# Performance work log

Measured on AMD Instinct MI355X. Metric: run time of the kernel, lower is better.

The kernel has to match this reference:

```python
import jax, jax.numpy as jnp
import numpy as np

B, S, E, H = 2, 2048, 1024, 16
HD = E // H

def setup_inputs() -> dict:
    key = jax.random.key(0)
    ks = jax.random.split(key, 9)
    s = 1.0 / np.sqrt(E)
    inp = {
        'x': jax.random.normal(ks[0], (B, S, E), dtype=jnp.float32),
        'Wq': jax.random.uniform(ks[1], (E, E), jnp.float32, -s, s),
        'bq': jax.random.uniform(ks[2], (E,), jnp.float32, -s, s),
        'Wk': jax.random.uniform(ks[3], (E, E), jnp.float32, -s, s),
        'bk': jax.random.uniform(ks[4], (E,), jnp.float32, -s, s),
        'Wv': jax.random.uniform(ks[5], (E, E), jnp.float32, -s, s),
        'bv': jax.random.uniform(ks[6], (E,), jnp.float32, -s, s),
        'Wo': jax.random.uniform(ks[7], (E, E), jnp.float32, -s, s),
        'bo': jax.random.uniform(ks[8], (E,), jnp.float32, -s, s),
    }
    return inp

def reference(x, Wq, bq, Wk, bk, Wv, bv, Wo, bo):
    # Linear layers: y = x @ W^T + b (torch nn.Linear convention)
    q = x @ Wq.T + bq  # [B,S,E]
    k = x @ Wk.T + bk
    v = x @ Wv.T + bv
    q = q.reshape(B, S, H, HD).transpose(0, 2, 1, 3)  # [B,H,S,hd]
    k = k.reshape(B, S, H, HD).transpose(0, 2, 1, 3)
    v = v.reshape(B, S, H, HD).transpose(0, 2, 1, 3)
    scores = jnp.einsum('bhqd,bhkd->bhqk', q, k) / jnp.sqrt(jnp.float32(HD))
    attn = jax.nn.softmax(scores, axis=-1)
    out = jnp.einsum('bhqk,bhkd->bhqd', attn, v)  # [B,H,S,hd]
    out = out.transpose(0, 2, 1, 3).reshape(B, S, E)
    return out @ Wo.T + bo
```

## Files before the change

### kernel.cpp

```cpp
#include <hip/hip_runtime.h>
#include <hip/hip_bf16.h>

#define B_ 2
#define S_ 2048
#define E_ 1024
#define H_ 16
#define HD_ 64
#define M_ (B_ * S_)

typedef __attribute__((ext_vector_type(8))) short bf16x8;
typedef __attribute__((ext_vector_type(4))) float f32x4;
typedef __attribute__((ext_vector_type(4))) unsigned short u16x4;
typedef unsigned short ushort_t;

static __device__ __forceinline__ ushort_t f2bf(float f) {
    union { __hip_bfloat16 b; ushort_t u; } cv;
    cv.b = __float2bfloat16(f);
    return cv.u;
}
static __device__ __forceinline__ float bf2f(ushort_t u) {
    union { unsigned int i; float f; } cv;
    cv.i = ((unsigned int)u) << 16;
    return cv.f;
}
static __device__ __forceinline__ void gl2lds16(const ushort_t* g, ushort_t* l) {
    __builtin_amdgcn_global_load_lds(
        (const __attribute__((address_space(1))) unsigned int*)g,
        (__attribute__((address_space(3))) unsigned int*)l,
        16, 0, 0);
}

__global__ __launch_bounds__(256)
void conv_pack(const float* __restrict__ x,  const float* __restrict__ Wq,
               const float* __restrict__ Wk, const float* __restrict__ Wv,
               const float* __restrict__ Wo, const float* __restrict__ bq,
               const float* __restrict__ bk, const float* __restrict__ bv,
               ushort_t* __restrict__ xb,  ushort_t* __restrict__ Wqb,
               ushort_t* __restrict__ Wkb, ushort_t* __restrict__ Wvb,
               ushort_t* __restrict__ Wohi, ushort_t* __restrict__ Wolo,
               float* __restrict__ bcat)
{
    const int NX = (B_ * S_ * E_) / 4;
    const int NW = (E_ * E_) / 4;
    const int total = NX + 4 * NW + 768;
    for (int u = blockIdx.x * blockDim.x + threadIdx.x; u < total;
         u += gridDim.x * blockDim.x) {
        if (u < NX) {
            float4 v = ((const float4*)x)[u];
            u16x4 o = { f2bf(v.x), f2bf(v.y), f2bf(v.z), f2bf(v.w) };
            ((u16x4*)xb)[u] = o;
        } else if (u < NX + 3 * NW) {
            int r = (u - NX) >> 18;
            int i = (u - NX) & (NW - 1);
            const float* src = (r == 0) ? Wq : ((r == 1) ? Wk : Wv);
            ushort_t*    dst = (r == 0) ? Wqb : ((r == 1) ? Wkb : Wvb);
            float4 v = ((const float4*)src)[i];
            u16x4 o = { f2bf(v.x), f2bf(v.y), f2bf(v.z), f2bf(v.w) };
            ((u16x4*)dst)[i] = o;
        } else if (u < NX + 4 * NW) {
            int i = u - NX - 3 * NW;
            float4 v = ((const float4*)Wo)[i];
            u16x4 hv, lv;
            float vv[4] = { v.x, v.y, v.z, v.w };
            #pragma unroll
            for (int r = 0; r < 4; ++r) {
                ushort_t hb = f2bf(vv[r]);
                hv[r] = hb;
                lv[r] = f2bf(vv[r] - bf2f(hb));
            }
            ((u16x4*)Wohi)[i] = hv;
            ((u16x4*)Wolo)[i] = lv;
        } else {
            int i = u - NX - 4 * NW;
            int r = i >> 8, ii = i & 255;
            const float* src = (r == 0) ? bq : ((r == 1) ? bk : bv);
            ((float4*)bcat)[r * 256 + ii] = ((const float4*)src)[ii];
        }
    }
}

template<int MODE>
__global__ __launch_bounds__(256)
void gemm_mfma(const ushort_t* __restrict__ Aa, const ushort_t* __restrict__ Ab,
               const ushort_t* __restrict__ W0p, const ushort_t* __restrict__ W1p,
               const ushort_t* __restrict__ W2p, const float* __restrict__ bias,
               ushort_t* __restrict__ O0, ushort_t* __restrict__ O1,
               ushort_t* __restrict__ O2, float* __restrict__ Of)
{
    constexpr int NBX = MODE ? 16 : 48;
    constexpr int NT  = MODE ? 48 : 16;
    __shared__ ushort_t As[2][128 * 64];
    __shared__ ushort_t Ws[2][64 * 64];

    const int nwg = NBX * (M_ / 128);
    const int b0  = blockIdx.x;
    const int bid = (b0 & 7) * (nwg >> 3) + (b0 >> 3);
    const int bx = bid % NBX, by = bid / NBX;
    const int m0 = by * 128, n0 = bx * 64;

    const int t = threadIdx.x;
    const int w = t >> 6, lane = t & 63;
    const int g = lane >> 4, qi = lane & 15, sw = qi & 7;
    const int wr = w >> 1, wc = w & 1;

    const ushort_t* WA;
    int nw0;
    int region = 0;
    if (MODE == 0) {
        region = n0 >> 10;
        WA = (region == 0) ? W0p : (region == 1) ? W1p : W2p;
        nw0 = n0 & 1023;
    } else {
        WA = W0p;
        nw0 = n0;
    }

    auto stage = [&](int buf, int kt) {
        const ushort_t *Acur, *Wcur;
        if (MODE == 0) { Acur = Aa; Wcur = WA; }
        else {
            int pass = kt >> 4;
            Acur = (pass == 2) ? Ab : Aa;
            Wcur = (pass == 1) ? W1p : W0p;
        }
        const int k0 = (MODE ? (kt & 15) : kt) * 64;
        #pragma unroll
        for (int it = 0; it < 4; ++it) {
            int idx = (it * 4 + w) * 64 + lane;
            int row = idx >> 3, c8 = idx & 7;
            gl2lds16(&Acur[(size_t)(m0 + row) * E_ + k0 + ((c8 ^ (row & 7)) << 3)],
                     &As[buf][(it * 4 + w) * 512]);
        }
        #pragma unroll
        for (int it = 0; it < 2; ++it) {
            int idx = (it * 4 + w) * 64 + lane;
            int row = idx >> 3, c8 = idx & 7;
            gl2lds16(&Wcur[(size_t)(nw0 + row) * E_ + k0 + ((c8 ^ (row & 7)) << 3)],
                     &Ws[buf][(it * 4 + w) * 512]);
        }
    };

    f32x4 acc[4][2];
    #pragma unroll
    for (int i = 0; i < 4; ++i)
        #pragma unroll
        for (int j = 0; j < 2; ++j) acc[i][j] = (f32x4){0.f, 0.f, 0.f, 0.f};

    stage(0, 0);
    __syncthreads();

    for (int kt = 0; kt < NT; ++kt) {
        const int cur = kt & 1;
        if (kt + 1 < NT) stage(cur ^ 1, kt + 1);
        #pragma unroll
        for (int h = 0; h < 2; ++h) {
            bf16x8 af[4], wf[2];
            #pragma unroll
            for (int i = 0; i < 4; ++i)
                af[i] = *(const bf16x8*)&As[cur][(wr * 64 + i * 16 + qi) * 64 +
                                                 (((h * 4 + g) ^ sw) << 3)];
            #pragma unroll
            for (int j = 0; j < 2; ++j)
                wf[j] = *(const bf16x8*)&Ws[cur][(wc * 32 + j * 16 + qi) * 64 +
                                                 (((h * 4 + g) ^ sw) << 3)];
            __builtin_amdgcn_s_setprio(1);
            #pragma unroll
            for (int i = 0; i < 4; ++i)
                #pragma unroll
                for (int j = 0; j < 2; ++j)
                    acc[i][j] = __builtin_amdgcn_mfma_f32_16x16x32_bf16(
                        af[i], wf[j], acc[i][j], 0, 0, 0);
            __builtin_amdgcn_s_setprio(0);
        }
        __syncthreads();
    }

    if (MODE == 0) {
        ushort_t* Out = (region == 0) ? O0 : (region == 1) ? O1 : O2;
        const float oscale = (region == 0) ? 0.18033688f : 1.0f;
        const int hh = (n0 & 1023) >> 6;
        #pragma unroll
        for (int j = 0; j < 2; ++j) {
            const int n = n0 + wc * 32 + j * 16 + qi;
            const int d = n & 63;
            const float bj = bias[n];
            #pragma unroll
            for (int i = 0; i < 4; ++i)
                #pragma unroll
                for (int r = 0; r < 4; ++r) {
                    const int m = m0 + wr * 64 + i * 16 + g * 4 + r;
                    const int b = m >> 11, s = m & (S_ - 1);
                    Out[(((size_t)(b * H_ + hh)) * S_ + s) * HD_ + d] =
                        f2bf((acc[i][j][r] + bj) * oscale);
                }
        }
    } else {
        #pragma unroll
        for (int j = 0; j < 2; ++j) {
            const int n = n0 + wc * 32 + j * 16 + qi;
            const float bj = bias[n];
            #pragma unroll
            for (int i = 0; i < 4; ++i)
                #pragma unroll
                for (int r = 0; r < 4; ++r) {
                    const int m = m0 + wr * 64 + i * 16 + g * 4 + r;
                    Of[(size_t)m * E_ + n] = acc[i][j][r] + bj;
                }
        }
    }
}

__global__ __launch_bounds__(256)
void attn_mfma(const ushort_t* __restrict__ Qg, const ushort_t* __restrict__ Kg,
               const ushort_t* __restrict__ Vg,
               ushort_t* __restrict__ Ohi, ushort_t* __restrict__ Olo)
{
    __shared__ ushort_t Ks[2][64][64];
    __shared__ ushort_t VtT[2][64][64];
    __shared__ ushort_t Ps[4][32][64];

    const int t    = threadIdx.x;
    const int w    = t >> 6;
    const int lane = t & 63;
    const int g    = lane >> 4;
    const int qi   = lane & 15;
    const int sw   = qi & 7;
    const int bh   = blockIdx.y;
    const int q0   = blockIdx.x * 128;
    const size_t base = (size_t)bh * S_ * HD_;
    const int kvg = t >> 4, dg = t & 15;

    auto stageK = [&](int buf, int tile) {
        const size_t nb = base + (size_t)tile * 64 * HD_;
        #pragma unroll
        for (int it = 0; it < 2; ++it) {
            int u = w * 128 + it * 64 + lane;
            int row = u >> 3, c8 = u & 7;
            gl2lds16(&Kg[nb + (size_t)row * HD_ + ((c8 ^ (row & 7)) << 3)],
                     &Ks[buf][0][0] + (size_t)(w * 128 + it * 64) * 8);
        }
    };

    bf16x8 qf[2][2];
    #pragma unroll
    for (int qc = 0; qc < 2; ++qc)
        #pragma unroll
        for (int h = 0; h < 2; ++h)
            qf[qc][h] = *(const bf16x8*)&Qg[base +
                (size_t)(q0 + w * 32 + qc * 16 + qi) * HD_ + (h * 4 + g) * 8];

    stageK(0, 0);
    {
        u16x4 vv[4];
        #pragma unroll
        for (int j = 0; j < 4; ++j)
            vv[j] = *(const u16x4*)&Vg[base + (size_t)(kvg * 4 + j) * HD_ + dg * 4];
        #pragma unroll
        for (int i = 0; i < 4; ++i) {
            int d = dg * 4 + i;
            u16x4 wvec = { vv[0][i], vv[1][i], vv[2][i], vv[3][i] };
            *(u16x4*)&VtT[0][d][8 * ((kvg >> 1) ^ (d & 7)) + 4 * (kvg & 1)] = wvec;
        }
    }
    __syncthreads();

    float m_run[2] = { -3.0e38f, -3.0e38f };
    float l_run[2] = { 0.f, 0.f };
    f32x4 oacc[2][4];
    #pragma unroll
    for (int qc = 0; qc < 2; ++qc)
        #pragma unroll
        for (int rb = 0; rb < 4; ++rb) oacc[qc][rb] = (f32x4){0.f, 0.f, 0.f, 0.f};

    for (int tile = 0; tile < S_ / 64; ++tile) {
        const int cur = tile & 1;
        const bool has_next = (tile + 1 < S_ / 64);

        u16x4 vpre[4];
        if (has_next) {
            stageK(cur ^ 1, tile + 1);
            const size_t nb = base + (size_t)(tile + 1) * 64 * HD_;
            #pragma unroll
            for (int j = 0; j < 4; ++j)
                vpre[j] = *(const u16x4*)&Vg[nb + (size_t)(kvg * 4 + j) * HD_ + dg * 4];
        }

        f32x4 sacc[2][4];
        #pragma unroll
        for (int rb = 0; rb < 4; ++rb) {
            bf16x8 ka0 = *(const bf16x8*)&Ks[cur][rb * 16 + qi][8 * ((0 + g) ^ sw)];
            bf16x8 ka1 = *(const bf16x8*)&Ks[cur][rb * 16 + qi][8 * ((4 + g) ^ sw)];
            #pragma unroll
            for (int qc = 0; qc < 2; ++qc) {
                f32x4 z = (f32x4){0.f, 0.f, 0.f, 0.f};
                z = __builtin_amdgcn_mfma_f32_16x16x32_bf16(ka0, qf[qc][0], z, 0, 0, 0);
                z = __builtin_amdgcn_mfma_f32_16x16x32_bf16(ka1, qf[qc][1], z, 0, 0, 0);
                sacc[qc][rb] = z;
            }
        }

        #pragma unroll
        for (int qc = 0; qc < 2; ++qc) {
            float smax = sacc[qc][0][0];
            #pragma unroll
            for (int rb = 0; rb < 4; ++rb)
                #pragma unroll
                for (int r = 0; r < 4; ++r) smax = fmaxf(smax, sacc[qc][rb][r]);
            smax = fmaxf(smax, __shfl_xor(smax, 16));
            smax = fmaxf(smax, __shfl_xor(smax, 32));
            const float mnew  = fmaxf(m_run[qc], smax);
            const float alpha = exp2f(m_run[qc] - mnew);
            float psum = 0.f;
            #pragma unroll
            for (int rb = 0; rb < 4; ++rb) {
                u16x4 pv;
                #pragma unroll
                for (int r = 0; r < 4; ++r) {
                    float p = exp2f(sacc[qc][rb][r] - mnew);
                    psum += p;
                    pv[r] = f2bf(p);
                }
                int ch = (2 * rb + (g >> 1)) ^ sw;
                *(u16x4*)&Ps[w][qc * 16 + qi][8 * ch + 4 * (g & 1)] = pv;
            }
            psum += __shfl_xor(psum, 16);
            psum += __shfl_xor(psum, 32);
            l_run[qc] = l_run[qc] * alpha + psum;
            m_run[qc] = mnew;
            #pragma unroll
            for (int rb = 0; rb < 4; ++rb)
                #pragma unroll
                for (int r = 0; r < 4; ++r) oacc[qc][rb][r] *= alpha;
        }

        #pragma unroll
        for (int kc = 0; kc < 2; ++kc) {
            bf16x8 pf0 = *(const bf16x8*)&Ps[w][qi][8 * ((4 * kc + g) ^ sw)];
            bf16x8 pf1 = *(const bf16x8*)&Ps[w][16 + qi][8 * ((4 * kc + g) ^ sw)];
            #pragma unroll
            for (int rb = 0; rb < 4; ++rb) {
                bf16x8 va = *(const bf16x8*)&VtT[cur][rb * 16 + qi][8 * ((4 * kc + g) ^ sw)];
                oacc[0][rb] = __builtin_amdgcn_mfma_f32_16x16x32_bf16(va, pf0, oacc[0][rb], 0, 0, 0);
                oacc[1][rb] = __builtin_amdgcn_mfma_f32_16x16x32_bf16(va, pf1, oacc[1][rb], 0, 0, 0);
            }
        }

        if (has_next) {
            #pragma unroll
            for (int i = 0; i < 4; ++i) {
                int d = dg * 4 + i;
                u16x4 wvec = { vpre[0][i], vpre[1][i], vpre[2][i], vpre[3][i] };
                *(u16x4*)&VtT[cur ^ 1][d][8 * ((kvg >> 1) ^ (d & 7)) + 4 * (kvg & 1)] = wvec;
            }
        }
        __syncthreads();
    }

    const int b = bh >> 4, h = bh & 15;
    #pragma unroll
    for (int qc = 0; qc < 2; ++qc) {
        const float inv = 1.f / l_run[qc];
        const size_t orow =
            (size_t)(b * S_ + q0 + w * 32 + qc * 16 + qi) * E_ + h * HD_;
        #pragma unroll
        for (int rb = 0; rb < 4; ++rb) {
            u16x4 hv, lv;
            #pragma unroll
            for (int r = 0; r < 4; ++r) {
                float v = oacc[qc][rb][r] * inv;
                ushort_t hb = f2bf(v);
                hv[r] = hb;
                lv[r] = f2bf(v - bf2f(hb));
            }
            *(u16x4*)&Ohi[orow + rb * 16 + g * 4] = hv;
            *(u16x4*)&Olo[orow + rb * 16 + g * 4] = lv;
        }
    }
}

extern "C" void kernel_launch(void* const* d_in, const int* in_sizes, int n_in,
                              void* d_out, int out_size, void* d_ws, size_t ws_size,
                              hipStream_t stream) {
    const float* x  = (const float*)d_in[0];
    const float* Wq = (const float*)d_in[1];
    const float* bq = (const float*)d_in[2];
    const float* Wk = (const float*)d_in[3];
    const float* bk = (const float*)d_in[4];
    const float* Wv = (const float*)d_in[5];
    const float* bv = (const float*)d_in[6];
    const float* Wo = (const float*)d_in[7];
    const float* bo = (const float*)d_in[8];
    float* out = (float*)d_out;

    const size_t T4 = (size_t)B_ * S_ * E_;
    const size_t W1 = (size_t)E_ * E_;
    ushort_t* xb   = (ushort_t*)d_ws;
    ushort_t* Wqb  = xb   + T4;
    ushort_t* Wkb  = Wqb  + W1;
    ushort_t* Wvb  = Wkb  + W1;
    ushort_t* Wohi = Wvb  + W1;
    ushort_t* Wolo = Wohi + W1;
    ushort_t* qws  = Wolo + W1;
    ushort_t* kws  = qws  + T4;
    ushort_t* vws  = kws  + T4;
    ushort_t* aohi = vws  + T4;
    ushort_t* aolo = aohi + T4;
    float*    bcat = (float*)(aolo + T4);

    dim3 blk(256);
    conv_pack<<<2048, blk, 0, stream>>>(x, Wq, Wk, Wv, Wo, bq, bk, bv,
                                        xb, Wqb, Wkb, Wvb, Wohi, Wolo, bcat);

    gemm_mfma<0><<<48 * 32, blk, 0, stream>>>(xb, nullptr, Wqb, Wkb, Wvb, bcat,
                                              qws, kws, vws, nullptr);

    dim3 ga(S_ / 128, B_ * H_);
    attn_mfma<<<ga, blk, 0, stream>>>(qws, kws, vws, aohi, aolo);

    gemm_mfma<1><<<16 * 32, blk, 0, stream>>>(aohi, aolo, Wohi, Wolo, nullptr, bo,
                                              nullptr, nullptr, nullptr, out);
}
```

Before: 262.2 us.

## Switch to fp16 MFMA, split-K attention, lazy rescale, drop hi/lo out-projection

Moves all operands from bf16 to fp16 and drops the hi/lo split of the attention output and Wo, so the output projection runs a third as many K passes. The QKV GEMM switches to 128x128 tiles with a single LDS buffer. Attention is split into two KV halves across a new grid dimension and merged by a new combine kernel. The online softmax now rescales only when the running max grows by more than a threshold. The risks are fp16 range and precision loss, plus an extra kernel launch and an extra round trip of partial outputs through memory.

```diff
diff --git a/kernel.cpp b/kernel.cpp
--- a/kernel.cpp
+++ b/kernel.cpp
@@ -1,5 +1,4 @@
 #include <hip/hip_runtime.h>
-#include <hip/hip_bf16.h>
 
 #define B_ 2
 #define S_ 2048
@@ -7,21 +6,20 @@
 #define H_ 16
 #define HD_ 64
 #define M_ (B_ * S_)
-
-typedef __attribute__((ext_vector_type(8))) short bf16x8;
+#define BH_ (B_ * H_)
+#define NROWS (BH_ * S_)
+
+typedef __attribute__((ext_vector_type(8))) _Float16 half8;
 typedef __attribute__((ext_vector_type(4))) float f32x4;
 typedef __attribute__((ext_vector_type(4))) unsigned short u16x4;
+typedef __attribute__((ext_vector_type(8))) unsigned short u16x8;
 typedef unsigned short ushort_t;
 
-static __device__ __forceinline__ ushort_t f2bf(float f) {
-    union { __hip_bfloat16 b; ushort_t u; } cv;
-    cv.b = __float2bfloat16(f);
-    return cv.u;
-}
-static __device__ __forceinline__ float bf2f(ushort_t u) {
-    union { unsigned int i; float f; } cv;
-    cv.i = ((unsigned int)u) << 16;
-    return cv.f;
+static __device__ __forceinline__ ushort_t f2h(float f) {
+    union { _Float16 h; ushort_t u; } c; c.h = (_Float16)f; return c.u;
+}
+static __device__ __forceinline__ float h2f(ushort_t u) {
+    union { _Float16 h; ushort_t u; } c; c.u = u; return (float)c.h;
 }
 static __device__ __forceinline__ void gl2lds16(const ushort_t* g, ushort_t* l) {
     __builtin_amdgcn_global_load_lds(
@@ -35,10 +33,9 @@
                const float* __restrict__ Wk, const float* __restrict__ Wv,
                const float* __restrict__ Wo, const float* __restrict__ bq,
                const float* __restrict__ bk, const float* __restrict__ bv,
-               ushort_t* __restrict__ xb,  ushort_t* __restrict__ Wqb,
-               ushort_t* __restrict__ Wkb, ushort_t* __restrict__ Wvb,
-               ushort_t* __restrict__ Wohi, ushort_t* __restrict__ Wolo,
-               float* __restrict__ bcat)
+               ushort_t* __restrict__ xh,  ushort_t* __restrict__ Wqh,
+               ushort_t* __restrict__ Wkh, ushort_t* __restrict__ Wvh,
+               ushort_t* __restrict__ Woh, float* __restrict__ bcat)
 {
     const int NX = (B_ * S_ * E_) / 4;
     const int NW = (E_ * E_) / 4;
@@ -47,95 +44,149 @@
          u += gridDim.x * blockDim.x) {
         if (u < NX) {
             float4 v = ((const float4*)x)[u];
-            u16x4 o = { f2bf(v.x), f2bf(v.y), f2bf(v.z), f2bf(v.w) };
-            ((u16x4*)xb)[u] = o;
-        } else if (u < NX + 3 * NW) {
+            u16x4 o = { f2h(v.x), f2h(v.y), f2h(v.z), f2h(v.w) };
+            ((u16x4*)xh)[u] = o;
+        } else if (u < NX + 4 * NW) {
             int r = (u - NX) >> 18;
             int i = (u - NX) & (NW - 1);
-            const float* src = (r == 0) ? Wq : ((r == 1) ? Wk : Wv);
-            ushort_t*    dst = (r == 0) ? Wqb : ((r == 1) ? Wkb : Wvb);
+            const float* src = (r == 0) ? Wq : (r == 1) ? Wk : (r == 2) ? Wv : Wo;
+            ushort_t*    dst = (r == 0) ? Wqh : (r == 1) ? Wkh : (r == 2) ? Wvh : Woh;
             float4 v = ((const float4*)src)[i];
-            u16x4 o = { f2bf(v.x), f2bf(v.y), f2bf(v.z), f2bf(v.w) };
+            u16x4 o = { f2h(v.x), f2h(v.y), f2h(v.z), f2h(v.w) };
             ((u16x4*)dst)[i] = o;
-        } else if (u < NX + 4 * NW) {
-            int i = u - NX - 3 * NW;
-            float4 v = ((const float4*)Wo)[i];
-            u16x4 hv, lv;
-            float vv[4] = { v.x, v.y, v.z, v.w };
-            #pragma unroll
-            for (int r = 0; r < 4; ++r) {
-                ushort_t hb = f2bf(vv[r]);
-                hv[r] = hb;
-                lv[r] = f2bf(vv[r] - bf2f(hb));
-            }
-            ((u16x4*)Wohi)[i] = hv;
-            ((u16x4*)Wolo)[i] = lv;
         } else {
             int i = u - NX - 4 * NW;
             int r = i >> 8, ii = i & 255;
-            const float* src = (r == 0) ? bq : ((r == 1) ? bk : bv);
+            const float* src = (r == 0) ? bq : (r == 1) ? bk : bv;
             ((float4*)bcat)[r * 256 + ii] = ((const float4*)src)[ii];
         }
     }
 }
 
-template<int MODE>
 __global__ __launch_bounds__(256)
-void gemm_mfma(const ushort_t* __restrict__ Aa, const ushort_t* __restrict__ Ab,
-               const ushort_t* __restrict__ W0p, const ushort_t* __restrict__ W1p,
-               const ushort_t* __restrict__ W2p, const float* __restrict__ bias,
-               ushort_t* __restrict__ O0, ushort_t* __restrict__ O1,
-               ushort_t* __restrict__ O2, float* __restrict__ Of)
+void gemm_qkv(const ushort_t* __restrict__ Ah, const ushort_t* __restrict__ W0p,
+              const ushort_t* __restrict__ W1p, const ushort_t* __restrict__ W2p,
+              const float* __restrict__ bias,
+              ushort_t* __restrict__ O0, ushort_t* __restrict__ O1,
+              ushort_t* __restrict__ O2)
 {
-    constexpr int NBX = MODE ? 16 : 48;
-    constexpr int NT  = MODE ? 48 : 16;
-    __shared__ ushort_t As[2][128 * 64];
-    __shared__ ushort_t Ws[2][64 * 64];
-
-    const int nwg = NBX * (M_ / 128);
+    __shared__ ushort_t As[128 * 64];
+    __shared__ ushort_t Ws[128 * 64];
+
+    const int nwg = 24 * 32;
     const int b0  = blockIdx.x;
     const int bid = (b0 & 7) * (nwg >> 3) + (b0 >> 3);
-    const int bx = bid % NBX, by = bid / NBX;
-    const int m0 = by * 128, n0 = bx * 64;
+    const int bx = bid % 24, by = bid / 24;
+    const int m0 = by * 128, n0 = bx * 128;
 
     const int t = threadIdx.x;
     const int w = t >> 6, lane = t & 63;
     const int g = lane >> 4, qi = lane & 15, sw = qi & 7;
     const int wr = w >> 1, wc = w & 1;
 
-    const ushort_t* WA;
-    int nw0;
-    int region = 0;
-    if (MODE == 0) {
-        region = n0 >> 10;
-        WA = (region == 0) ? W0p : (region == 1) ? W1p : W2p;
-        nw0 = n0 & 1023;
-    } else {
-        WA = W0p;
-        nw0 = n0;
-    }
-
-    auto stage = [&](int buf, int kt) {
-        const ushort_t *Acur, *Wcur;
-        if (MODE == 0) { Acur = Aa; Wcur = WA; }
-        else {
-            int pass = kt >> 4;
-            Acur = (pass == 2) ? Ab : Aa;
-            Wcur = (pass == 1) ? W1p : W0p;
-        }
-        const int k0 = (MODE ? (kt & 15) : kt) * 64;
+    const int region = n0 >> 10;
+    const ushort_t* WA = (region == 0) ? W0p : (region == 1) ? W1p : W2p;
+    const int nw0 = n0 & 1023;
+
+    f32x4 acc[4][4];
+    #pragma unroll
+    for (int i = 0; i < 4; ++i)
+        #pragma unroll
+        for (int j = 0; j < 4; ++j) acc[i][j] = (f32x4){0.f, 0.f, 0.f, 0.f};
+
+    for (int kt = 0; kt < 16; ++kt) {
+        __syncthreads();
+        const int k0 = kt * 64;
         #pragma unroll
         for (int it = 0; it < 4; ++it) {
             int idx = (it * 4 + w) * 64 + lane;
             int row = idx >> 3, c8 = idx & 7;
-            gl2lds16(&Acur[(size_t)(m0 + row) * E_ + k0 + ((c8 ^ (row & 7)) << 3)],
+            gl2lds16(&Ah[(size_t)(m0 + row) * E_ + k0 + ((c8 ^ (row & 7)) << 3)],
+                     &As[(it * 4 + w) * 512]);
+        }
+        #pragma unroll
+        for (int it = 0; it < 4; ++it) {
+            int idx = (it * 4 + w) * 64 + lane;
+            int row = idx >> 3, c8 = idx & 7;
+            gl2lds16(&WA[(size_t)(nw0 + row) * E_ + k0 + ((c8 ^ (row & 7)) << 3)],
+                     &Ws[(it * 4 + w) * 512]);
+        }
+        __syncthreads();
+
+        #pragma unroll
+        for (int h = 0; h < 2; ++h) {
+            half8 af[4], wf[4];
+            #pragma unroll
+            for (int i = 0; i < 4; ++i)
+                af[i] = *(const half8*)&As[(wr * 64 + i * 16 + qi) * 64 +
+                                           (((h * 4 + g) ^ sw) << 3)];
+            #pragma unroll
+            for (int j = 0; j < 4; ++j)
+                wf[j] = *(const half8*)&Ws[(wc * 64 + j * 16 + qi) * 64 +
+                                           (((h * 4 + g) ^ sw) << 3)];
+            __builtin_amdgcn_s_setprio(1);
+            #pragma unroll
+            for (int i = 0; i < 4; ++i)
+                #pragma unroll
+                for (int j = 0; j < 4; ++j)
+                    acc[i][j] = __builtin_amdgcn_mfma_f32_16x16x32_f16(
+                        af[i], wf[j], acc[i][j], 0, 0, 0);
+            __builtin_amdgcn_s_setprio(0);
+        }
+    }
+
+    ushort_t* Out = (region == 0) ? O0 : (region == 1) ? O1 : O2;
+    const float osc = (region == 0) ? 0.18033688f : 1.0f;
+    #pragma unroll
+    for (int j = 0; j < 4; ++j) {
+        const int n = n0 + wc * 64 + j * 16 + qi;
+        const int nn = n & 1023;
+        const int hh = nn >> 6, d = nn & 63;
+        const float bj = bias[n];
+        #pragma unroll
+        for (int i = 0; i < 4; ++i)
+            #pragma unroll
+            for (int r = 0; r < 4; ++r) {
+                const int m = m0 + wr * 64 + i * 16 + g * 4 + r;
+                const int b = m >> 11, s = m & (S_ - 1);
+                Out[(((size_t)(b * H_ + hh)) * S_ + s) * HD_ + d] =
+                    f2h((acc[i][j][r] + bj) * osc);
+            }
+    }
+}
+
+__global__ __launch_bounds__(256)
+void gemm_out(const ushort_t* __restrict__ Ah, const ushort_t* __restrict__ Wh,
+              const float* __restrict__ bo, float* __restrict__ Of)
+{
+    __shared__ ushort_t As[2][128 * 64];
+    __shared__ ushort_t Ws[2][64 * 64];
+
+    const int nwg = 16 * 32;
+    const int b0  = blockIdx.x;
+    const int bid = (b0 & 7) * (nwg >> 3) + (b0 >> 3);
+    const int bx = bid % 16, by = bid / 16;
+    const int m0 = by * 128, n0 = bx * 64;
+
+    const int t = threadIdx.x;
+    const int w = t >> 6, lane = t & 63;
+    const int g = lane >> 4, qi = lane & 15, sw = qi & 7;
+    const int wr = w >> 1, wc = w & 1;
+
+    auto stage = [&](int buf, int kt) {
+        const int k0 = kt * 64;
+        #pragma unroll
+        for (int it = 0; it < 4; ++it) {
+            int idx = (it * 4 + w) * 64 + lane;
+            int row = idx >> 3, c8 = idx & 7;
+            gl2lds16(&Ah[(size_t)(m0 + row) * E_ + k0 + ((c8 ^ (row & 7)) << 3)],
                      &As[buf][(it * 4 + w) * 512]);
         }
         #pragma unroll
         for (int it = 0; it < 2; ++it) {
             int idx = (it * 4 + w) * 64 + lane;
             int row = idx >> 3, c8 = idx & 7;
-            gl2lds16(&Wcur[(size_t)(nw0 + row) * E_ + k0 + ((c8 ^ (row & 7)) << 3)],
+            gl2lds16(&Wh[(size_t)(n0 + row) * E_ + k0 + ((c8 ^ (row & 7)) << 3)],
                      &Ws[buf][(it * 4 + w) * 512]);
         }
     };
@@ -149,71 +200,50 @@
     stage(0, 0);
     __syncthreads();
 
-    for (int kt = 0; kt < NT; ++kt) {
+    for (int kt = 0; kt < 16; ++kt) {
         const int cur = kt & 1;
-        if (kt + 1 < NT) stage(cur ^ 1, kt + 1);
+        if (kt + 1 < 16) stage(cur ^ 1, kt + 1);
         #pragma unroll
         for (int h = 0; h < 2; ++h) {
-            bf16x8 af[4], wf[2];
+            half8 af[4], wf[2];
             #pragma unroll
             for (int i = 0; i < 4; ++i)
-                af[i] = *(const bf16x8*)&As[cur][(wr * 64 + i * 16 + qi) * 64 +
-                                                 (((h * 4 + g) ^ sw) << 3)];
+                af[i] = *(const half8*)&As[cur][(wr * 64 + i * 16 + qi) * 64 +
+                                                (((h * 4 + g) ^ sw) << 3)];
             #pragma unroll
             for (int j = 0; j < 2; ++j)
-                wf[j] = *(const bf16x8*)&Ws[cur][(wc * 32 + j * 16 + qi) * 64 +
-                                                 (((h * 4 + g) ^ sw) << 3)];
+                wf[j] = *(const half8*)&Ws[cur][(wc * 32 + j * 16 + qi) * 64 +
+                                                (((h * 4 + g) ^ sw) << 3)];
             __builtin_amdgcn_s_setprio(1);
             #pragma unroll
             for (int i = 0; i < 4; ++i)
                 #pragma unroll
                 for (int j = 0; j < 2; ++j)
-                    acc[i][j] = __builtin_amdgcn_mfma_f32_16x16x32_bf16(
+                    acc[i][j] = __builtin_amdgcn_mfma_f32_16x16x32_f16(
                         af[i], wf[j], acc[i][j], 0, 0, 0);
             __builtin_amdgcn_s_setprio(0);
         }
         __syncthreads();
     }
 
-    if (MODE == 0) {
-        ushort_t* Out = (region == 0) ? O0 : (region == 1) ? O1 : O2;
-        const float oscale = (region == 0) ? 0.18033688f : 1.0f;
-        const int hh = (n0 & 1023) >> 6;
-        #pragma unroll
-        for (int j = 0; j < 2; ++j) {
-            const int n = n0 + wc * 32 + j * 16 + qi;
-            const int d = n & 63;
-            const float bj = bias[n];
-            #pragma unroll
-            for (int i = 0; i < 4; ++i)
-                #pragma unroll
-                for (int r = 0; r < 4; ++r) {
-                    const int m = m0 + wr * 64 + i * 16 + g * 4 + r;
-                    const int b = m >> 11, s = m & (S_ - 1);
-                    Out[(((size_t)(b * H_ + hh)) * S_ + s) * HD_ + d] =
-                        f2bf((acc[i][j][r] + bj) * oscale);
-                }
-        }
-    } else {
-        #pragma unroll
-        for (int j = 0; j < 2; ++j) {
-            const int n = n0 + wc * 32 + j * 16 + qi;
-            const float bj = bias[n];
-            #pragma unroll
-            for (int i = 0; i < 4; ++i)
-                #pragma unroll
-                for (int r = 0; r < 4; ++r) {
-                    const int m = m0 + wr * 64 + i * 16 + g * 4 + r;
-                    Of[(size_t)m * E_ + n] = acc[i][j][r] + bj;
-                }
-        }
+    #pragma unroll
+    for (int j = 0; j < 2; ++j) {
+        const int n = n0 + wc * 32 + j * 16 + qi;
+        const float bj = bo[n];
+        #pragma unroll
+        for (int i = 0; i < 4; ++i)
+            #pragma unroll
+            for (int r = 0; r < 4; ++r) {
+                const int m = m0 + wr * 64 + i * 16 + g * 4 + r;
+                Of[(size_t)m * E_ + n] = acc[i][j][r] + bj;
+            }
     }
 }
 
 __global__ __launch_bounds__(256)
 void attn_mfma(const ushort_t* __restrict__ Qg, const ushort_t* __restrict__ Kg,
                const ushort_t* __restrict__ Vg,
-               ushort_t* __restrict__ Ohi, ushort_t* __restrict__ Olo)
+               ushort_t* __restrict__ On, float2* __restrict__ ml)
 {
     __shared__ ushort_t Ks[2][64][64];
     __shared__ ushort_t VtT[2][64][64];
@@ -227,6 +257,8 @@
     const int sw   = qi & 7;
     const int bh   = blockIdx.y;
     const int q0   = blockIdx.x * 128;
+    const int z    = blockIdx.z;
+    const int t0   = z * 16, t1 = t0 + 16;
     const size_t base = (size_t)bh * S_ * HD_;
     const int kvg = t >> 4, dg = t & 15;
 
@@ -241,20 +273,21 @@
         }
     };
 
-    bf16x8 qf[2][2];
+    half8 qf[2][2];
     #pragma unroll
     for (int qc = 0; qc < 2; ++qc)
         #pragma unroll
         for (int h = 0; h < 2; ++h)
-            qf[qc][h] = *(const bf16x8*)&Qg[base +
+            qf[qc][h] = *(const half8*)&Qg[base +
                 (size_t)(q0 + w * 32 + qc * 16 + qi) * HD_ + (h * 4 + g) * 8];
 
-    stageK(0, 0);
+    stageK(0, t0);
     {
+        const size_t nb = base + (size_t)t0 * 64 * HD_;
         u16x4 vv[4];
         #pragma unroll
         for (int j = 0; j < 4; ++j)
-            vv[j] = *(const u16x4*)&Vg[base + (size_t)(kvg * 4 + j) * HD_ + dg * 4];
+            vv[j] = *(const u16x4*)&Vg[nb + (size_t)(kvg * 4 + j) * HD_ + dg * 4];
         #pragma unroll
         for (int i = 0; i < 4; ++i) {
             int d = dg * 4 + i;
@@ -272,9 +305,9 @@
         #pragma unroll
         for (int rb = 0; rb < 4; ++rb) oacc[qc][rb] = (f32x4){0.f, 0.f, 0.f, 0.f};
 
-    for (int tile = 0; tile < S_ / 64; ++tile) {
+    for (int tile = t0; tile < t1; ++tile) {
         const int cur = tile & 1;
-        const bool has_next = (tile + 1 < S_ / 64);
+        const bool has_next = (tile + 1 < t1);
 
         u16x4 vpre[4];
         if (has_next) {
@@ -288,14 +321,14 @@
         f32x4 sacc[2][4];
         #pragma unroll
         for (int rb = 0; rb < 4; ++rb) {
-            bf16x8 ka0 = *(const bf16x8*)&Ks[cur][rb * 16 + qi][8 * ((0 + g) ^ sw)];
-            bf16x8 ka1 = *(const bf16x8*)&Ks[cur][rb * 16 + qi][8 * ((4 + g) ^ sw)];
+            half8 ka0 = *(const half8*)&Ks[cur][rb * 16 + qi][8 * ((0 + g) ^ sw)];
+            half8 ka1 = *(const half8*)&Ks[cur][rb * 16 + qi][8 * ((4 + g) ^ sw)];
             #pragma unroll
             for (int qc = 0; qc < 2; ++qc) {
-                f32x4 z = (f32x4){0.f, 0.f, 0.f, 0.f};
-                z = __builtin_amdgcn_mfma_f32_16x16x32_bf16(ka0, qf[qc][0], z, 0, 0, 0);
-                z = __builtin_amdgcn_mfma_f32_16x16x32_bf16(ka1, qf[qc][1], z, 0, 0, 0);
-                sacc[qc][rb] = z;
+                f32x4 zz = (f32x4){0.f, 0.f, 0.f, 0.f};
+                zz = __builtin_amdgcn_mfma_f32_16x16x32_f16(ka0, qf[qc][0], zz, 0, 0, 0);
+                zz = __builtin_amdgcn_mfma_f32_16x16x32_f16(ka1, qf[qc][1], zz, 0, 0, 0);
+                sacc[qc][rb] = zz;
             }
         }
 
@@ -308,40 +341,43 @@
                 for (int r = 0; r < 4; ++r) smax = fmaxf(smax, sacc[qc][rb][r]);
             smax = fmaxf(smax, __shfl_xor(smax, 16));
             smax = fmaxf(smax, __shfl_xor(smax, 32));
-            const float mnew  = fmaxf(m_run[qc], smax);
-            const float alpha = exp2f(m_run[qc] - mnew);
+            if (__any(smax > m_run[qc] + 8.0f)) {
+                const float mnew  = fmaxf(m_run[qc], smax);
+                const float alpha = exp2f(m_run[qc] - mnew);
+                l_run[qc] *= alpha;
+                #pragma unroll
+                for (int rb = 0; rb < 4; ++rb)
+                    #pragma unroll
+                    for (int r = 0; r < 4; ++r) oacc[qc][rb][r] *= alpha;
+                m_run[qc] = mnew;
+            }
             float psum = 0.f;
             #pragma unroll
             for (int rb = 0; rb < 4; ++rb) {
                 u16x4 pv;
                 #pragma unroll
                 for (int r = 0; r < 4; ++r) {
-                    float p = exp2f(sacc[qc][rb][r] - mnew);
+                    float p = exp2f(sacc[qc][rb][r] - m_run[qc]);
                     psum += p;
-                    pv[r] = f2bf(p);
+                    pv[r] = f2h(p);
                 }
                 int ch = (2 * rb + (g >> 1)) ^ sw;
                 *(u16x4*)&Ps[w][qc * 16 + qi][8 * ch + 4 * (g & 1)] = pv;
             }
             psum += __shfl_xor(psum, 16);
             psum += __shfl_xor(psum, 32);
-            l_run[qc] = l_run[qc] * alpha + psum;
-            m_run[qc] = mnew;
-            #pragma unroll
-            for (int rb = 0; rb < 4; ++rb)
-                #pragma unroll
-                for (int r = 0; r < 4; ++r) oacc[qc][rb][r] *= alpha;
+            l_run[qc] += psum;
         }
 
         #pragma unroll
         for (int kc = 0; kc < 2; ++kc) {
-            bf16x8 pf0 = *(const bf16x8*)&Ps[w][qi][8 * ((4 * kc + g) ^ sw)];
-            bf16x8 pf1 = *(const bf16x8*)&Ps[w][16 + qi][8 * ((4 * kc + g) ^ sw)];
+            half8 pf0 = *(const half8*)&Ps[w][qi][8 * ((4 * kc + g) ^ sw)];
+            half8 pf1 = *(const half8*)&Ps[w][16 + qi][8 * ((4 * kc + g) ^ sw)];
             #pragma unroll
             for (int rb = 0; rb < 4; ++rb) {
-                bf16x8 va = *(const bf16x8*)&VtT[cur][rb * 16 + qi][8 * ((4 * kc + g) ^ sw)];
-                oacc[0][rb] = __builtin_amdgcn_mfma_f32_16x16x32_bf16(va, pf0, oacc[0][rb], 0, 0, 0);
-                oacc[1][rb] = __builtin_amdgcn_mfma_f32_16x16x32_bf16(va, pf1, oacc[1][rb], 0, 0, 0);
+                half8 va = *(const half8*)&VtT[cur][rb * 16 + qi][8 * ((4 * kc + g) ^ sw)];
+                oacc[0][rb] = __builtin_amdgcn_mfma_f32_16x16x32_f16(va, pf0, oacc[0][rb], 0, 0, 0);
+                oacc[1][rb] = __builtin_amdgcn_mfma_f32_16x16x32_f16(va, pf1, oacc[1][rb], 0, 0, 0);
             }
         }
 
@@ -356,25 +392,54 @@
         __syncthreads();
     }
 
+    #pragma unroll
+    for (int qc = 0; qc < 2; ++qc) {
+        const int qrow = q0 + w * 32 + qc * 16 + qi;
+        const float inv = 1.f / l_run[qc];
+        const size_t orow = (size_t)z * NROWS * HD_ +
+                            ((size_t)bh * S_ + qrow) * HD_;
+        #pragma unroll
+        for (int rb = 0; rb < 4; ++rb) {
+            u16x4 ov;
+            #pragma unroll
+            for (int r = 0; r < 4; ++r) ov[r] = f2h(oacc[qc][rb][r] * inv);
+            *(u16x4*)&On[orow + rb * 16 + g * 4] = ov;
+        }
+        if (g == 0) {
+            float2 v; v.x = m_run[qc]; v.y = l_run[qc];
+            ml[(size_t)z * NROWS + (size_t)bh * S_ + qrow] = v;
+        }
+    }
+}
+
+__global__ __launch_bounds__(256)
+void attn_combine(const ushort_t* __restrict__ On, const float2* __restrict__ ml,
+                  ushort_t* __restrict__ aoh)
+{
+    const int gid = blockIdx.x * 256 + threadIdx.x;
+    const int row = gid >> 2, dp = gid & 3;
+    float2 a = ml[row];
+    float2 b2 = ml[NROWS + row];
+    const float Mx = fmaxf(a.x, b2.x);
+    const float w1 = a.y * exp2f(a.x - Mx);
+    const float w2 = b2.y * exp2f(b2.x - Mx);
+    const float inv = 1.f / (w1 + w2);
+    const float c1 = w1 * inv, c2 = w2 * inv;
+
+    const size_t o1 = (size_t)row * HD_ + dp * 16;
+    const size_t o2 = (size_t)NROWS * HD_ + o1;
+    const int bh = row >> 11, s = row & (S_ - 1);
     const int b = bh >> 4, h = bh & 15;
-    #pragma unroll
-    for (int qc = 0; qc < 2; ++qc) {
-        const float inv = 1.f / l_run[qc];
-        const size_t orow =
-            (size_t)(b * S_ + q0 + w * 32 + qc * 16 + qi) * E_ + h * HD_;
-        #pragma unroll
-        for (int rb = 0; rb < 4; ++rb) {
-            u16x4 hv, lv;
-            #pragma unroll
-            for (int r = 0; r < 4; ++r) {
-                float v = oacc[qc][rb][r] * inv;
-                ushort_t hb = f2bf(v);
-                hv[r] = hb;
-                lv[r] = f2bf(v - bf2f(hb));
-            }
-            *(u16x4*)&Ohi[orow + rb * 16 + g * 4] = hv;
-            *(u16x4*)&Olo[orow + rb * 16 + g * 4] = lv;
-        }
+    ushort_t* dst = &aoh[((size_t)(b * S_ + s)) * E_ + h * HD_ + dp * 16];
+    #pragma unroll
+    for (int c = 0; c < 2; ++c) {
+        u16x8 v1 = *(const u16x8*)&On[o1 + c * 8];
+        u16x8 v2 = *(const u16x8*)&On[o2 + c * 8];
+        u16x8 o;
+        #pragma unroll
+        for (int e = 0; e < 8; ++e)
+            o[e] = f2h(c1 * h2f(v1[e]) + c2 * h2f(v2[e]));
+        *(u16x8*)&dst[c * 8] = o;
     }
 }
 
@@ -394,29 +459,29 @@
 
     const size_t T4 = (size_t)B_ * S_ * E_;
     const size_t W1 = (size_t)E_ * E_;
-    ushort_t* xb   = (ushort_t*)d_ws;
-    ushort_t* Wqb  = xb   + T4;
-    ushort_t* Wkb  = Wqb  + W1;
-    ushort_t* Wvb  = Wkb  + W1;
-    ushort_t* Wohi = Wvb  + W1;
-    ushort_t* Wolo = Wohi + W1;
-    ushort_t* qws  = Wolo + W1;
-    ushort_t* kws  = qws  + T4;
-    ushort_t* vws  = kws  + T4;
-    ushort_t* aohi = vws  + T4;
-    ushort_t* aolo = aohi + T4;
-    float*    bcat = (float*)(aolo + T4);
+    ushort_t* xh  = (ushort_t*)d_ws;
+    ushort_t* Wqh = xh  + T4;
+    ushort_t* Wkh = Wqh + W1;
+    ushort_t* Wvh = Wkh + W1;
+    ushort_t* Woh = Wvh + W1;
+    ushort_t* qh  = Woh + W1;
+    ushort_t* kh  = qh  + T4;
+    ushort_t* vh  = kh  + T4;
+    ushort_t* On  = vh  + T4;
+    float2*   ml  = (float2*)(On + 2 * T4);
+    float*    bcat = (float*)(ml + 2 * NROWS);
+    ushort_t* aoh = xh;
 
     dim3 blk(256);
     conv_pack<<<2048, blk, 0, stream>>>(x, Wq, Wk, Wv, Wo, bq, bk, bv,
-                                        xb, Wqb, Wkb, Wvb, Wohi, Wolo, bcat);
-
-    gemm_mfma<0><<<48 * 32, blk, 0, stream>>>(xb, nullptr, Wqb, Wkb, Wvb, bcat,
-                                              qws, kws, vws, nullptr);
-
-    dim3 ga(S_ / 128, B_ * H_);
-    attn_mfma<<<ga, blk, 0, stream>>>(qws, kws, vws, aohi, aolo);
-
-    gemm_mfma<1><<<16 * 32, blk, 0, stream>>>(aohi, aolo, Wohi, Wolo, nullptr, bo,
-                                              nullptr, nullptr, nullptr, out);
-}
+                                        xh, Wqh, Wkh, Wvh, Woh, bcat);
+
+    gemm_qkv<<<24 * 32, blk, 0, stream>>>(xh, Wqh, Wkh, Wvh, bcat, qh, kh, vh);
+
+    dim3 ga(S_ / 128, BH_, 2);
+    attn_mfma<<<ga, blk, 0, stream>>>(qh, kh, vh, On, ml);
+
+    attn_combine<<<(NROWS * 4) / 256, blk, 0, stream>>>(On, ml, aoh);
+
+    gemm_out<<<16 * 32, blk, 0, stream>>>(aoh, Woh, bo, out);
+}
```

Measured after the change: 238.1 us. 9.2% less time.
